# Performance work log

Measured on AMD Instinct MI355X. Metric: run time of the kernel, lower is better.

## Reference

```python
import jax, jax.numpy as jnp
import numpy as np

B, T = 64, 20
VOCAB, E, CE, ANS = 20000, 300, 1024, 3000
H, N, W, R = 512, 256, 64, 4
RW = R * W
IF_SIZES = [RW, R, W, 1, W, W, R, 1, 1, 3 * R]  # read_keys, read_str, write_key, write_str, erase, write_vec, free, alloc_g, write_g, modes
IF_TOT = sum(IF_SIZES)
CLIP = 20.0
EPS = 1e-6


def _cosine_weights(mem, keys, strengths):
    # mem [B,N,W], keys [B,K,W], strengths [B,K] -> softmax over N
    mem_n = mem / (jnp.linalg.norm(mem, axis=-1, keepdims=True) + EPS)
    key_n = keys / (jnp.linalg.norm(keys, axis=-1, keepdims=True) + EPS)
    sim = jnp.einsum('bkw,bnw->bkn', key_n, mem_n)
    return jax.nn.softmax(sim * strengths[..., None], axis=-1)


def _init_state(b):
    z = lambda *s: jnp.zeros(s, jnp.float32)
    return (z(b, N, W), z(b, N, N), z(b, N), z(b, R, N), z(b, N), z(b, N), z(b, R, W), z(b, H), z(b, H))


def _dnc_step(Wih, Whh, b, Wif, bif, Wout, bout, state, x):
    mem, link, prec, wr, ww, usage, rvec, h, c = state
    bsz = x.shape[0]
    inp = jnp.concatenate([x, rvec.reshape(bsz, RW)], -1)
    gates = inp @ Wih + h @ Whh + b
    gi, gf, gg, go = jnp.split(gates, 4, -1)
    c = jax.nn.sigmoid(gf) * c + jax.nn.sigmoid(gi) * jnp.tanh(gg)
    h = jax.nn.sigmoid(go) * jnp.tanh(c)
    hc = jnp.clip(h, -CLIP, CLIP)
    xi = hc @ Wif + bif
    p = jnp.split(xi, np.cumsum(IF_SIZES)[:-1].tolist(), axis=-1)
    read_keys = jnp.tanh(p[0]).reshape(bsz, R, W)
    read_str = jax.nn.softplus(p[1])
    write_key = jnp.tanh(p[2]).reshape(bsz, 1, W)
    write_str = jax.nn.softplus(p[3])
    erase = jax.nn.sigmoid(p[4])
    write_vec = jnp.tanh(p[5])
    free = jax.nn.sigmoid(p[6])
    alloc_g = jax.nn.sigmoid(p[7])
    write_g = jax.nn.sigmoid(p[8])
    modes = jax.nn.softmax(p[9].reshape(bsz, R, 3), -1)

    # usage update and allocation (sort-based, data dependent)
    psi = jnp.prod(1.0 - free[..., None] * wr, axis=1)          # [B,N]
    usage = (usage + ww - usage * ww) * psi
    s_idx = jnp.argsort(usage, axis=-1)                          # ascending usage
    s_u = jnp.take_along_axis(usage, s_idx, -1)
    cp = jnp.cumprod(jnp.concatenate([jnp.ones_like(s_u[:, :1]), s_u[:, :-1]], -1), -1)
    a_sorted = (1.0 - s_u) * cp
    inv = jnp.argsort(s_idx, axis=-1)
    alloc = jnp.take_along_axis(a_sorted, inv, -1)

    # write
    cw = _cosine_weights(mem, write_key, write_str)[:, 0]        # [B,N]
    ww = write_g * (alloc_g * alloc + (1.0 - alloc_g) * cw)
    mem = mem * (1.0 - ww[..., None] * erase[:, None, :]) + ww[..., None] * write_vec[:, None, :]

    # temporal link matrix
    link = (1.0 - ww[:, :, None] - ww[:, None, :]) * link + ww[:, :, None] * prec[:, None, :]
    link = link * (1.0 - jnp.eye(N, dtype=link.dtype))
    prec = (1.0 - ww.sum(-1, keepdims=True)) * prec + ww

    # read
    fw = jnp.einsum('bij,brj->bri', link, wr)
    bw = jnp.einsum('bji,brj->bri', link, wr)
    cr = _cosine_weights(mem, read_keys, read_str)
    wr = modes[..., 0:1] * bw + modes[..., 1:2] * cr + modes[..., 2:3] * fw
    rvec = jnp.einsum('brn,bnw->brw', wr, mem)

    out = jnp.concatenate([hc, rvec.reshape(bsz, RW)], -1) @ Wout + bout
    out = jnp.clip(out, -CLIP, CLIP)
    return (mem, link, prec, wr, ww, usage, rvec, h, c), out


def _model(img_feat, emb, img_W, img_b, q_Wih, q_Whh, q_b, q_Wif, q_bif, q_Wout, q_bout,
           c_Wih, c_Whh, c_b, c_Wif, c_bif, c_Wout, c_bout, fc1_W, fc1_b, fc2_W, fc2_b, qst):
    bsz = qst.shape[0]
    # question encoder: embedding -> tanh -> DNC over time -> mean pool
    qv = jnp.tanh(emb[qst])                                      # [B,T,E]
    step = lambda st, x: _dnc_step(q_Wih, q_Whh, q_b, q_Wif, q_bif, q_Wout, q_bout, st, x)
    _, outs = jax.lax.scan(step, _init_state(bsz), jnp.swapaxes(qv, 0, 1))
    qfeat = outs.mean(0)                                         # [B,CE]
    # image encoder: fc on frozen VGG feature, L2 norm (norm detached)
    imgf = img_feat @ img_W + img_b
    imgf = imgf / jax.lax.stop_gradient(jnp.linalg.norm(imgf, axis=1, keepdims=True))
    comb = jnp.tanh(imgf * qfeat)
    # controller DNC: single timestep
    st_c, out_c = _dnc_step(c_Wih, c_Whh, c_b, c_Wif, c_bif, c_Wout, c_bout, _init_state(bsz), comb)
    rv_c = st_c[6].reshape(bsz, RW)
    last = jnp.tanh(jnp.concatenate([out_c, rv_c], -1))
    last = jnp.tanh(last @ fc1_W + fc1_b)
    return last @ fc2_W + fc2_b                                  # logits [B,ANS]


def setup_inputs():
    ks = jax.random.split(jax.random.key(0), 20)
    g = lambda k, s, sc=0.05: jax.random.normal(k, s, dtype=jnp.float32) * sc
    z = lambda *s: jnp.zeros(s, jnp.float32)
    return {
        'img_feat': g(ks[0], (B, 4096), 1.0),
        'qst': jax.random.randint(ks[1], (B, T), 0, VOCAB),
        'emb': g(ks[2], (VOCAB, E)),
        'img_W': g(ks[3], (4096, CE)), 'img_b': z(CE),
        'q_Wih': g(ks[4], (E + RW, 4 * H)), 'q_Whh': g(ks[5], (H, 4 * H)), 'q_b': z(4 * H),
        'q_Wif': g(ks[6], (H, IF_TOT)), 'q_bif': z(IF_TOT),
        'q_Wout': g(ks[7], (H + RW, CE)), 'q_bout': z(CE),
        'c_Wih': g(ks[8], (CE + RW, 4 * H)), 'c_Whh': g(ks[9], (H, 4 * H)), 'c_b': z(4 * H),
        'c_Wif': g(ks[10], (H, IF_TOT)), 'c_bif': z(IF_TOT),
        'c_Wout': g(ks[11], (H + RW, CE)), 'c_bout': z(CE),
        'fc1_W': g(ks[12], (CE + RW, ANS)), 'fc1_b': z(ANS),
        'fc2_W': g(ks[13], (ANS, ANS)), 'fc2_b': z(ANS),
    }


def reference(img_feat, qst, emb, img_W, img_b, q_Wih, q_Whh, q_b, q_Wif, q_bif, q_Wout, q_bout,
              c_Wih, c_Whh, c_b, c_Wif, c_bif, c_Wout, c_bout, fc1_W, fc1_b, fc2_W, fc2_b):
    return _model(img_feat, emb, img_W, img_b, q_Wih, q_Whh, q_b, q_Wif, q_bif, q_Wout, q_bout,
                  c_Wih, c_Whh, c_b, c_Wif, c_bif, c_Wout, c_bout, fc1_W, fc1_b, fc2_W, fc2_b, qst)
```

## Files before the change

kernel.cpp:

```cpp
#include <hip/hip_runtime.h>
#include <cmath>

#define CLIPV 20.0f
#define EPSV 1e-6f

__device__ __forceinline__ float sigmoidf_(float x){ return 1.0f/(1.0f + expf(-x)); }
__device__ __forceinline__ float softplusf_(float x){ return (x > 20.0f) ? x : log1pf(expf(x)); }
__device__ __forceinline__ float clipf_(float x){ return fminf(fmaxf(x, -CLIPV), CLIPV); }

__device__ __forceinline__ float wave_sum64(float v){
  #pragma unroll
  for (int off=32; off>=1; off>>=1) v += __shfl_xor(v, off, 64);
  return v;
}
__device__ __forceinline__ float wave_max64(float v){
  #pragma unroll
  for (int off=32; off>=1; off>>=1) v = fmaxf(v, __shfl_xor(v, off, 64));
  return v;
}
__device__ __forceinline__ float block_sum256(float v, float* s_red){
  v = wave_sum64(v);
  __syncthreads();
  if ((threadIdx.x & 63) == 0) s_red[threadIdx.x>>6] = v;
  __syncthreads();
  return s_red[0]+s_red[1]+s_red[2]+s_red[3];
}
__device__ __forceinline__ float block_max256(float v, float* s_red){
  v = wave_max64(v);
  __syncthreads();
  if ((threadIdx.x & 63) == 0) s_red[threadIdx.x>>6] = v;
  __syncthreads();
  return fmaxf(fmaxf(s_red[0],s_red[1]), fmaxf(s_red[2],s_red[3]));
}

__device__ __forceinline__ void cstore(float* p, float v){
  __hip_atomic_store(p, v, __ATOMIC_RELAXED, __HIP_MEMORY_SCOPE_AGENT);
}

#define WS_MEM    0
#define WS_LINK   1048576
#define WS_PREC   5242880
#define WS_WR     5275648
#define WS_WW     5341184
#define WS_USAGE  5357568
#define WS_BAR    5373952
#define WS_ZONEA  5374976
#define WS_QSUM   5374976
#define WS_HTS    5440512
#define WS_RVS    6128640
#define WS_XIS    6472704
#define WS_GXP    7105728
#define WS_ZONEC  9727168
#define WS_IMGF   10879168
#define WS_COMB   10944704
#define WS_LASTB  11010240
#define WS_HID1   11092160
#define WS_QV     11284160

__global__ void embed_kernel(const int* __restrict__ qst, const float* __restrict__ emb,
                             float* __restrict__ qv){
  int idx = blockIdx.x*256 + threadIdx.x;
  if (idx >= 1280*300) return;
  int m = idx / 300;
  int e = idx - m*300;
  int t = m >> 6, b = m & 63;
  int tok = qst[b*20 + t];
  qv[idx] = tanhf(emb[(size_t)tok*300 + e]);
}

__global__ __launch_bounds__(256) void gemm64(
    int M, int N, int Ktot, int KS,
    const float* __restrict__ A, int lda,
    const float* __restrict__ B,
    const float* __restrict__ bias,
    float* __restrict__ out, float* __restrict__ part, int mode)
{
  __shared__ float As[32*68];
  __shared__ float Bs[32*68];
  int tid = threadIdx.x;
  int nb = blockIdx.x*64, ks = blockIdx.y, mb = blockIdx.z*64;
  int Kc = (((Ktot + KS - 1)/KS) + 3) & ~3;
  int kbeg = ks*Kc, kend = min(Ktot, kbeg + Kc);
  int tm = tid >> 4, tn = tid & 15;
  float acc[4][4];
  #pragma unroll
  for (int i=0;i<4;i++){ acc[i][0]=0.f; acc[i][1]=0.f; acc[i][2]=0.f; acc[i][3]=0.f; }

  for (int k0 = kbeg; k0 < kend; k0 += 32){
    int klim = kend - k0; if (klim > 32) klim = 32;
    #pragma unroll
    for (int i=0;i<2;i++){
      int idx = tid + i*256;
      int m = idx >> 3, kq = (idx & 7) << 2;
      if (kq < klim){
        const float* ap = A + (size_t)(mb+m)*lda + k0 + kq;
        float4 v;
        if (kq + 3 < klim) v = *(const float4*)ap;
        else { v.x=ap[0]; v.y=(kq+1<klim)?ap[1]:0.f; v.z=(kq+2<klim)?ap[2]:0.f; v.w=0.f; }
        float* as = As + m;
        as[(kq+0)*68]=v.x; as[(kq+1)*68]=v.y; as[(kq+2)*68]=v.z; as[(kq+3)*68]=v.w;
      }
    }
    #pragma unroll
    for (int i=0;i<2;i++){
      int idx = tid + i*256;
      int kk = idx >> 4, nq = (idx & 15) << 2;
      int n = nb + nq;
      float4 v = {0.f,0.f,0.f,0.f};
      if (kk < klim && n < N){
        const float* bp = B + (size_t)(k0+kk)*N + n;
        if (n + 3 < N) v = *(const float4*)bp;
        else { v.x=bp[0]; v.y=(n+1<N)?bp[1]:0.f; v.z=(n+2<N)?bp[2]:0.f; }
      }
      *(float4*)(Bs + kk*68 + nq) = v;
    }
    __syncthreads();
    for (int kk = 0; kk < klim; kk++){
      float4 a = *(const float4*)(As + kk*68 + tm*4);
      float4 bv = *(const float4*)(Bs + kk*68 + tn*4);
      acc[0][0]+=a.x*bv.x; acc[0][1]+=a.x*bv.y; acc[0][2]+=a.x*bv.z; acc[0][3]+=a.x*bv.w;
      acc[1][0]+=a.y*bv.x; acc[1][1]+=a.y*bv.y; acc[1][2]+=a.y*bv.z; acc[1][3]+=a.y*bv.w;
      acc[2][0]+=a.z*bv.x; acc[2][1]+=a.z*bv.y; acc[2][2]+=a.z*bv.z; acc[2][3]+=a.z*bv.w;
      acc[3][0]+=a.w*bv.x; acc[3][1]+=a.w*bv.y; acc[3][2]+=a.w*bv.z; acc[3][3]+=a.w*bv.w;
    }
    __syncthreads();
  }

  #pragma unroll
  for (int i=0;i<4;i++){
    int m = tm*4 + i;
    #pragma unroll
    for (int j=0;j<4;j++){
      int n = nb + tn*4 + j;
      if (n < N){
        if (mode == 0){
          part[((size_t)(ks*64 + m))*N + n] = acc[i][j];
        } else {
          float v = acc[i][j] + (bias ? bias[n] : 0.f);
          if (mode == 2) v = tanhf(v);
          out[(size_t)(mb+m)*N + n] = v;
        }
      }
    }
  }
}

__global__ void reduce64(const float* __restrict__ part, int KS, int MN4, int N,
                         const float* __restrict__ bias, float* __restrict__ out, int mode){
  int idx = blockIdx.x*256 + threadIdx.x;
  if (idx >= MN4) return;
  int base = idx*4;
  int n = base % N;
  float4 s = {0.f,0.f,0.f,0.f};
  size_t stride = (size_t)MN4*4;
  for (int p=0;p<KS;p++){
    float4 t = *(const float4*)(part + (size_t)p*stride + base);
    s.x+=t.x; s.y+=t.y; s.z+=t.z; s.w+=t.w;
  }
  if (bias){
    float4 bb = *(const float4*)(bias + n);
    s.x+=bb.x; s.y+=bb.y; s.z+=bb.z; s.w+=bb.w;
  }
  if (mode == 1){ s.x=tanhf(s.x); s.y=tanhf(s.y); s.z=tanhf(s.z); s.w=tanhf(s.w); }
  *(float4*)(out + base) = s;
}

__global__ __launch_bounds__(256) void comb_kernel(const float* __restrict__ imgf,
                                                   const float* __restrict__ qsum,
                                                   float* __restrict__ comb){
  __shared__ float s_red[4];
  int b = blockIdx.x, tid = threadIdx.x;
  float ss = 0.f;
  for (int j = tid; j < 1024; j += 256){ float v = imgf[b*1024+j]; ss += v*v; }
  ss = wave_sum64(ss);
  if ((tid & 63) == 0) s_red[tid>>6] = ss;
  __syncthreads();
  float inv = 1.0f / sqrtf(s_red[0]+s_red[1]+s_red[2]+s_red[3]);
  for (int j = tid; j < 1024; j += 256)
    comb[b*1024+j] = tanhf(imgf[b*1024+j]*inv * qsum[b*1024+j]*0.05f);
}

__global__ void tanhrvec_kernel(const float* __restrict__ rvecT, float* __restrict__ lastB){
  int idx = blockIdx.x*256 + threadIdx.x;
  if (idx >= 16384) return;
  int b = idx & 63, i = idx >> 6;
  lastB[(size_t)b*1280 + 1024 + i] = tanhf(rvecT[i*64 + b]);
}

struct SD_t {
  float s_rk[256], s_rstr[4], s_wkey[64], s_erase[64], s_wvec[64];
  float s_free[4], s_modes[12], s_scal[3], s_pad0[1];
  float s_wr[1024];
  float s_wwnew[256], s_usage[256], s_prec[256], s_scan[256], s_sim[256];
  float s_C[1024], s_D[1024];
  float s_red[4], s_PQ[8];
};
struct SGLO_t { float red[4*768]; float g2[768]; };
struct Shm {
  float Wg[768*8];
  float Wo[768*4];
  float Wi[512*4];
  union { SGLO_t glo; SD_t d; } u;
};


__device__ __forceinline__ void gbar(int* subs, int* root, int* ggen, int epoch){
  __syncthreads();
  if (threadIdx.x == 0){
    asm volatile("s_waitcnt vmcnt(0)" ::: "memory");
    int g = blockIdx.x & 15;
    int old = __hip_atomic_fetch_add(&subs[g*16], 1, __ATOMIC_RELAXED, __HIP_MEMORY_SCOPE_AGENT);
    if (old == 16*epoch - 1){
      int r = __hip_atomic_fetch_add(root, 1, __ATOMIC_RELAXED, __HIP_MEMORY_SCOPE_AGENT);
      if (r == 16*epoch - 1){
        #pragma unroll
        for (int gg = 0; gg < 16; gg++)
          __hip_atomic_store(&ggen[gg*16], epoch, __ATOMIC_RELAXED, __HIP_MEMORY_SCOPE_AGENT);
      }
    }
    while (__hip_atomic_load(&ggen[g*16], __ATOMIC_RELAXED, __HIP_MEMORY_SCOPE_AGENT) < epoch)
      __builtin_amdgcn_s_sleep(2);
    asm volatile("" ::: "memory");
  }
  __syncthreads();
}

__global__ __launch_bounds__(256) void dnc_recur(
    int T, int outmode, int slot0,
    const float* __restrict__ xpart, const float* __restrict__ Wih_r,
    const float* __restrict__ Whh, const float* __restrict__ gb,
    const float* __restrict__ Wif, const float* __restrict__ bif,
    const float* __restrict__ Wout, const float* __restrict__ bout,
    float* __restrict__ ws, float* __restrict__ outbuf, int* __restrict__ barmem)
{
  __shared__ Shm sh;

  float* memS  = ws + WS_MEM;
  float* linkS = ws + WS_LINK;
  float* precB = ws + WS_PREC;
  float* wrS   = ws + WS_WR;
  float* wwS   = ws + WS_WW;
  float* usgS  = ws + WS_USAGE;
  float* htS   = ws + WS_HTS;
  float* rvS   = ws + WS_RVS;
  float* xiSl  = ws + WS_XIS;
  int* subs  = barmem;
  int* root  = barmem + 256;
  int* ggen  = barmem + 288;
  int* xict  = barmem + 576;
  int* subsH = barmem + 608;
  int* rootH = barmem + 896;

  int tid = threadIdx.x, bid = blockIdx.x;
  int lane = tid & 63, wid = tid >> 6;
  int b_ = tid & 63, q_ = tid >> 6;

  {
    int c2 = bid*2;
    float2* Wg2w = (float2*)sh.Wg;
    for (int e2 = tid; e2 < 3072; e2 += 256){
      int k = e2 >> 2, g = e2 & 3;
      const float* src = (k < 256) ? (Wih_r + (size_t)k*2048 + g*512 + c2)
                                   : (Whh + (size_t)(k-256)*2048 + g*512 + c2);
      Wg2w[e2] = *(const float2*)src;
    }
    int c4o = bid*4;
    float4* Wo4 = (float4*)sh.Wo;
    for (int k = tid; k < 768; k += 256)
      Wo4[k] = *(const float4*)(Wout + (size_t)k*1024 + c4o);
    if (bid < 118){
      for (int e = tid; e < 2048; e += 256){
        int k = e >> 2, c = e & 3;
        int col = c4o + c;
        sh.Wi[e] = (col < 471) ? Wif[(size_t)k*471 + col] : 0.f;
      }
    }
  }
  float bo = bout[bid*4 + q_];
  float bifv = 0.f;
  if (bid < 118 && bid*4 + q_ < 471) bifv = bif[bid*4 + q_];
  __syncthreads();

  float c_reg = 0.f;
  float qacc = 0.f;
  int epoch = 0;

  for (int t = 0; t < T; t++){
    int pp = t & 1, wp = (t + 1) & 1;

    {
      if (t > 0){
        float accG[8] = {0.f,0.f,0.f,0.f,0.f,0.f,0.f,0.f};
        float accO[4] = {0.f,0.f,0.f,0.f};
        const float* rvP = rvS + (size_t)(slot0+t-1)*16384;
        const float* hP  = htS + (size_t)(slot0+t-1)*32768;
        for (int c = 0; c < 12; c++){
          int k0 = c*64 + wid*16;
          bool isH = (k0 >= 256);
          const float* src = isH ? (hP + (size_t)(k0-256)*64) : (rvP + (size_t)k0*64);
          float a[16];
          #pragma unroll
          for (int u=0; u<16; u++) a[u] = src[u*64 + lane];
          #pragma unroll
          for (int u=0; u<16; u++){
            int k = k0 + u;
            float4 w0 = *(const float4*)(sh.Wg + (size_t)k*8);
            float4 w1 = *(const float4*)(sh.Wg + (size_t)k*8 + 4);
            int orow = isH ? (k - 256) : (512 + k);
            float4 wo = *(const float4*)(sh.Wo + (size_t)orow*4);
            float av = a[u];
            float ao = isH ? clipf_(av) : av;
            accG[0] += av*w0.x; accG[1] += av*w0.y; accG[2] += av*w0.z; accG[3] += av*w0.w;
            accG[4] += av*w1.x; accG[5] += av*w1.y; accG[6] += av*w1.z; accG[7] += av*w1.w;
            accO[0] += ao*wo.x; accO[1] += ao*wo.y; accO[2] += ao*wo.z; accO[3] += ao*wo.w;
          }
        }
        #pragma unroll
        for (int j=0;j<8;j++) sh.u.glo.red[wid*768 + j*64 + lane] = accG[j];
        #pragma unroll
        for (int j=0;j<4;j++) sh.u.glo.red[wid*768 + (8+j)*64 + lane] = accO[j];
      }
      __syncthreads();
      #pragma unroll
      for (int v=0; v<3; v++){
        int j = q_ + v*4;
        float s;
        if (j < 8){
          int col = (j>>1)*512 + bid*2 + (j&1);
          s = gb[col] + xpart[((size_t)(t*64 + b_))*2048 + col];
        } else {
          s = bo;
        }
        if (t > 0){
          s += sh.u.glo.red[0*768 + j*64 + b_];
          s += sh.u.glo.red[1*768 + j*64 + b_];
          s += sh.u.glo.red[2*768 + j*64 + b_];
          s += sh.u.glo.red[3*768 + j*64 + b_];
        }
        sh.u.glo.g2[j*64 + b_] = s;
      }
      __syncthreads();
      if (t > 0) qacc += clipf_(sh.u.glo.g2[(8+q_)*64 + b_]);
      if (tid < 128){
        int jj = q_;
        float gi = sh.u.glo.g2[(0+jj)*64 + b_];
        float gf = sh.u.glo.g2[(2+jj)*64 + b_];
        float gg = sh.u.glo.g2[(4+jj)*64 + b_];
        float go = sh.u.glo.g2[(6+jj)*64 + b_];
        float cn = sigmoidf_(gf)*c_reg + sigmoidf_(gi)*tanhf(gg);
        float hn = sigmoidf_(go)*tanhf(cn);
        c_reg = cn;
        int col = bid*2 + jj;
        cstore(&htS[(size_t)(slot0+t)*32768 + col*64 + b_], hn);
      }
    }

    __syncthreads();
    if (tid == 0){
      asm volatile("s_waitcnt vmcnt(0)" ::: "memory");
      int g = bid & 15;
      int old = __hip_atomic_fetch_add(&subsH[g*16], 1, __ATOMIC_RELAXED, __HIP_MEMORY_SCOPE_AGENT);
      if (old == 16*(t+1) - 1)
        __hip_atomic_fetch_add(rootH, 1, __ATOMIC_RELAXED, __HIP_MEMORY_SCOPE_AGENT);
    }

    if (bid < 118){
      if (tid == 0){
        while (__hip_atomic_load(rootH, __ATOMIC_RELAXED, __HIP_MEMORY_SCOPE_AGENT) < 16*(t+1))
          __builtin_amdgcn_s_sleep(1);
        asm volatile("" ::: "memory");
      }
      __syncthreads();
      float acc[4] = {0.f,0.f,0.f,0.f};
      const float* hP = htS + (size_t)(slot0+t)*32768;
      for (int c = 0; c < 8; c++){
        int k0 = c*64 + wid*16;
        float a[16];
        #pragma unroll
        for (int u=0; u<16; u++) a[u] = hP[(size_t)(k0+u)*64 + lane];
        #pragma unroll
        for (int u=0; u<16; u++){
          float4 wv = *(const float4*)(sh.Wi + (size_t)(k0+u)*4);
          float ac = clipf_(a[u]);
          acc[0] += ac*wv.x; acc[1] += ac*wv.y; acc[2] += ac*wv.z; acc[3] += ac*wv.w;
        }
      }
      #pragma unroll
      for (int j=0;j<4;j++) sh.u.glo.red[wid*256 + j*64 + lane] = acc[j];
      __syncthreads();
      {
        float s = bifv;
        #pragma unroll
        for (int w=0;w<4;w++) s += sh.u.glo.red[w*256 + q_*64 + b_];
        int col = bid*4 + q_;
        if (col < 471) cstore(&xiSl[(size_t)(slot0+t)*30144 + b_*471 + col], s);
      }
      __syncthreads();
      if (tid == 0)
        __hip_atomic_fetch_add(xict, 1, __ATOMIC_RELAXED, __HIP_MEMORY_SCOPE_AGENT);
    }

    if (bid < 64){
      SD_t& sd = sh.u.d;
      int b = bid;
      const float* prec_in  = precB + pp*16384;
      float*       prec_out = precB + wp*16384;

      for (int e = tid; e < 1024; e += 256){
        sd.s_wr[e] = wrS[(size_t)b*1024 + e];
        sd.s_C[e] = 0.f; sd.s_D[e] = 0.f;
      }
      float wwold = wwS[(size_t)b*256 + tid];
      sd.s_usage[tid] = usgS[(size_t)b*256 + tid];
      sd.s_prec[tid]  = prec_in[(size_t)b*256 + tid];

      if (tid == 0){
        while (__hip_atomic_load(xict, __ATOMIC_RELAXED, __HIP_MEMORY_SCOPE_AGENT) < 118*(t+1))
          __builtin_amdgcn_s_sleep(1);
        asm volatile("" ::: "memory");
      }
      __syncthreads();

      const float* xrow = xiSl + (size_t)(slot0+t)*30144 + (size_t)b*471;
      for (int idx = tid; idx < 471; idx += 256){
        float v = xrow[idx];
        if (idx < 256)       sd.s_rk[idx] = tanhf(v);
        else if (idx < 260)  sd.s_rstr[idx-256] = softplusf_(v);
        else if (idx < 324)  sd.s_wkey[idx-260] = v;
        else if (idx == 324) sd.s_scal[0] = softplusf_(v);
        else if (idx < 389)  sd.s_erase[idx-325] = sigmoidf_(v);
        else if (idx < 453)  sd.s_wvec[idx-389] = tanhf(v);
        else if (idx < 457)  sd.s_free[idx-453] = sigmoidf_(v);
        else if (idx == 457) sd.s_scal[1] = sigmoidf_(v);
        else if (idx == 458) sd.s_scal[2] = sigmoidf_(v);
        else                 sd.s_modes[idx-459] = v;
      }
      __syncthreads();

      if (tid < 4){
        float m0 = sd.s_modes[tid*3], m1 = sd.s_modes[tid*3+1], m2 = sd.s_modes[tid*3+2];
        float mx = fmaxf(m0, fmaxf(m1,m2));
        float e0 = expf(m0-mx), e1 = expf(m1-mx), e2 = expf(m2-mx);
        float s = e0+e1+e2;
        sd.s_modes[tid*3] = e0/s; sd.s_modes[tid*3+1] = e1/s; sd.s_modes[tid*3+2] = e2/s;
      }
      {
        float k = sd.s_rk[wid*64 + lane];
        float ss = wave_sum64(k*k);
        sd.s_rk[wid*64 + lane] = k / (sqrtf(ss) + EPSV);
      }
      if (wid == 0){
        float k = sd.s_wkey[lane];
        float ss = wave_sum64(k*k);
        sd.s_wkey[lane] = k / (sqrtf(ss) + EPSV);
      }

      {
        float psi = 1.f;
        #pragma unroll
        for (int r=0;r<4;r++) psi *= (1.f - sd.s_free[r]*sd.s_wr[r*256+tid]);
        float u = (sd.s_usage[tid] + wwold - sd.s_usage[tid]*wwold) * psi;
        sd.s_usage[tid] = u;
        usgS[(size_t)b*256 + tid] = u;
      }
      __syncthreads();

      int rank_r;
      {
        float u = sd.s_usage[tid];
        int rank = 0;
        #pragma unroll 4
        for (int j4=0;j4<256;j4+=4){
          float4 uv = *(const float4*)(sd.s_usage + j4);
          rank += (uv.x < u) || (uv.x == u && (j4+0) < tid);
          rank += (uv.y < u) || (uv.y == u && (j4+1) < tid);
          rank += (uv.z < u) || (uv.z == u && (j4+2) < tid);
          rank += (uv.w < u) || (uv.w == u && (j4+3) < tid);
        }
        rank_r = rank;
        sd.s_scan[rank] = u;
      }
      __syncthreads();

      for (int off=1; off<256; off<<=1){
        float tv = (tid >= off) ? sd.s_scan[tid-off] : 1.f;
        __syncthreads();
        sd.s_scan[tid] *= tv;
        __syncthreads();
      }
      float alloc_r;
      {
        float u = sd.s_usage[tid];
        float cpe = (rank_r > 0) ? sd.s_scan[rank_r-1] : 1.f;
        alloc_r = (1.f - u) * cpe;
      }

      {
        const float4* Mrow = (const float4*)(memS + (size_t)b*16384 + (size_t)tid*64);
        float nrm2 = 0.f, dt = 0.f;
        #pragma unroll
        for (int c4 = 0; c4 < 16; c4++){
          float4 mv = Mrow[c4];
          int w0 = c4*4;
          nrm2 += mv.x*mv.x + mv.y*mv.y + mv.z*mv.z + mv.w*mv.w;
          dt += mv.x*sd.s_wkey[w0] + mv.y*sd.s_wkey[w0+1] + mv.z*sd.s_wkey[w0+2] + mv.w*sd.s_wkey[w0+3];
        }
        sd.s_sim[tid] = dt / (sqrtf(nrm2)+EPSV) * sd.s_scal[0];
      }
      __syncthreads();

      {
        float v = sd.s_sim[tid];
        float mx = block_max256(v, sd.s_red);
        float e = expf(v - mx);
        float sm = block_sum256(e, sd.s_red);
        float cw = e / sm;
        float wwn = sd.s_scal[2] * (sd.s_scal[1]*alloc_r + (1.f - sd.s_scal[1])*cw);
        sd.s_wwnew[tid] = wwn;
        wwS[(size_t)b*256 + tid] = wwn;
        float wws = block_sum256(wwn, sd.s_red);
        prec_out[(size_t)b*256 + tid] = (1.f - wws)*sd.s_prec[tid] + wwn;
        #pragma unroll
        for (int r=0;r<4;r++){
          float pv  = block_sum256(sd.s_prec[tid]*sd.s_wr[r*256+tid], sd.s_red);
          float qv_ = block_sum256(wwn*sd.s_wr[r*256+tid], sd.s_red);
          if (tid == 0){ sd.s_PQ[r] = pv; sd.s_PQ[4+r] = qv_; }
        }
      }
      __syncthreads();

      float aA[4] = {0,0,0,0}, aB[4] = {0,0,0,0};
      {
        const float4* Lrow = (const float4*)(linkS + (size_t)b*65536 + (size_t)tid*256);
        for (int c4 = 0; c4 < 64; c4++){
          float4 lv = Lrow[c4];
          int j = c4*4;
          float w0n = sd.s_wwnew[j], w1n = sd.s_wwnew[j+1], w2n = sd.s_wwnew[j+2], w3n = sd.s_wwnew[j+3];
          #pragma unroll
          for (int r=0;r<4;r++){
            float wr0 = sd.s_wr[r*256+j], wr1 = sd.s_wr[r*256+j+1];
            float wr2 = sd.s_wr[r*256+j+2], wr3 = sd.s_wr[r*256+j+3];
            aA[r] += lv.x*wr0 + lv.y*wr1 + lv.z*wr2 + lv.w*wr3;
            aB[r] += lv.x*(w0n*wr0) + lv.y*(w1n*wr1) + lv.z*(w2n*wr2) + lv.w*(w3n*wr3);
          }
        }
      }
      __syncthreads();

      {
        int cg = tid & 63, ioff = tid >> 6;
        int j0 = cg*4;
        float wwj0 = sd.s_wwnew[j0], wwj1 = sd.s_wwnew[j0+1], wwj2 = sd.s_wwnew[j0+2], wwj3 = sd.s_wwnew[j0+3];
        float pj0 = sd.s_prec[j0], pj1 = sd.s_prec[j0+1], pj2 = sd.s_prec[j0+2], pj3 = sd.s_prec[j0+3];
        float cC[4][4] = {{0}}, cD[4][4] = {{0}};
        float4* Lb = (float4*)(linkS + (size_t)b*65536);
        for (int it = 0; it < 64; it++){
          int i = it*4 + ioff;
          float4 lv = Lb[(size_t)i*64 + cg];
          float wwi = sd.s_wwnew[i];
          float4 ln;
          ln.x = (1.f - wwi - wwj0)*lv.x + wwi*pj0;
          ln.y = (1.f - wwi - wwj1)*lv.y + wwi*pj1;
          ln.z = (1.f - wwi - wwj2)*lv.z + wwi*pj2;
          ln.w = (1.f - wwi - wwj3)*lv.w + wwi*pj3;
          if (i >= j0 && i < j0+4){
            if (i == j0)        ln.x = 0.f;
            else if (i == j0+1) ln.y = 0.f;
            else if (i == j0+2) ln.z = 0.f;
            else                ln.w = 0.f;
          }
          Lb[(size_t)i*64 + cg] = ln;
          #pragma unroll
          for (int r=0;r<4;r++){
            float wri = sd.s_wr[r*256+i];
            float vbi = wwi*wri;
            cC[r][0] += lv.x*wri; cC[r][1] += lv.y*wri; cC[r][2] += lv.z*wri; cC[r][3] += lv.w*wri;
            cD[r][0] += lv.x*vbi; cD[r][1] += lv.y*vbi; cD[r][2] += lv.z*vbi; cD[r][3] += lv.w*vbi;
          }
        }
        for (int w=0; w<4; w++){
          if (ioff == w){
            #pragma unroll
            for (int r=0;r<4;r++){
              sd.s_C[r*256+j0+0] += cC[r][0]; sd.s_C[r*256+j0+1] += cC[r][1];
              sd.s_C[r*256+j0+2] += cC[r][2]; sd.s_C[r*256+j0+3] += cC[r][3];
              sd.s_D[r*256+j0+0] += cD[r][0]; sd.s_D[r*256+j0+1] += cD[r][1];
              sd.s_D[r*256+j0+2] += cD[r][2]; sd.s_D[r*256+j0+3] += cD[r][3];
            }
          }
          __syncthreads();
        }
      }

      float pr[4];
      {
        float4* Mrow = (float4*)(memS + (size_t)b*16384 + (size_t)tid*64);
        float wwn = sd.s_wwnew[tid];
        float nrm2 = 0.f, d0=0.f, d1=0.f, d2=0.f, d3=0.f;
        #pragma unroll
        for (int c4 = 0; c4 < 16; c4++){
          float4 mv = Mrow[c4];
          int w0 = c4*4;
          mv.x = mv.x*(1.f - wwn*sd.s_erase[w0+0]) + wwn*sd.s_wvec[w0+0];
          mv.y = mv.y*(1.f - wwn*sd.s_erase[w0+1]) + wwn*sd.s_wvec[w0+1];
          mv.z = mv.z*(1.f - wwn*sd.s_erase[w0+2]) + wwn*sd.s_wvec[w0+2];
          mv.w = mv.w*(1.f - wwn*sd.s_erase[w0+3]) + wwn*sd.s_wvec[w0+3];
          Mrow[c4] = mv;
          nrm2 += mv.x*mv.x + mv.y*mv.y + mv.z*mv.z + mv.w*mv.w;
          d0 += mv.x*sd.s_rk[w0] + mv.y*sd.s_rk[w0+1] + mv.z*sd.s_rk[w0+2] + mv.w*sd.s_rk[w0+3];
          d1 += mv.x*sd.s_rk[64+w0] + mv.y*sd.s_rk[64+w0+1] + mv.z*sd.s_rk[64+w0+2] + mv.w*sd.s_rk[64+w0+3];
          d2 += mv.x*sd.s_rk[128+w0] + mv.y*sd.s_rk[128+w0+1] + mv.z*sd.s_rk[128+w0+2] + mv.w*sd.s_rk[128+w0+3];
          d3 += mv.x*sd.s_rk[192+w0] + mv.y*sd.s_rk[192+w0+1] + mv.z*sd.s_rk[192+w0+2] + mv.w*sd.s_rk[192+w0+3];
        }
        float inv = 1.f/(sqrtf(nrm2)+EPSV);
        pr[0] = d0*inv*sd.s_rstr[0];
        pr[1] = d1*inv*sd.s_rstr[1];
        pr[2] = d2*inv*sd.s_rstr[2];
        pr[3] = d3*inv*sd.s_rstr[3];
      }
      #pragma unroll
      for (int r=0;r<4;r++){
        float mx = block_max256(pr[r], sd.s_red);
        float e = expf(pr[r] - mx);
        float sm = block_sum256(e, sd.s_red);
        pr[r] = e/sm;
      }
      __syncthreads();

      {
        float wwn = sd.s_wwnew[tid], pn = sd.s_prec[tid];
        #pragma unroll
        for (int r=0;r<4;r++){
          float wro = sd.s_wr[r*256+tid];
          float fw  = (1.f-wwn)*aA[r] - aB[r] + wwn*(sd.s_PQ[r] - pn*wro);
          float bwv = (1.f-wwn)*sd.s_C[r*256+tid] - sd.s_D[r*256+tid] + pn*(sd.s_PQ[4+r] - wwn*wro);
          float wrn = sd.s_modes[r*3+0]*bwv + sd.s_modes[r*3+1]*pr[r] + sd.s_modes[r*3+2]*fw;
          wrS[(size_t)b*1024 + r*256 + tid] = wrn;
          sd.s_wr[r*256+tid] = wrn;
        }
      }
      __syncthreads();

      {
        int r = tid >> 6, w = tid & 63;
        const float* Mb = memS + (size_t)b*16384;
        float acc = 0.f;
        for (int n=0; n<256; n++) acc += sd.s_wr[r*256+n]*Mb[(size_t)n*64 + w];
        cstore(&rvS[(size_t)(slot0+t)*16384 + (r*64 + w)*64 + b], acc);
      }
    }

    epoch++; gbar(subs, root, ggen, epoch);
  }

  {
    float accO[4] = {0.f,0.f,0.f,0.f};
    const float* rvP = rvS + (size_t)(slot0+T-1)*16384;
    const float* hP  = htS + (size_t)(slot0+T-1)*32768;
    for (int c = 0; c < 12; c++){
      int k0 = c*64 + wid*16;
      bool isH = (k0 >= 256);
      const float* src = isH ? (hP + (size_t)(k0-256)*64) : (rvP + (size_t)k0*64);
      float a[16];
      #pragma unroll
      for (int u=0; u<16; u++) a[u] = src[u*64 + lane];
      #pragma unroll
      for (int u=0; u<16; u++){
        int k = k0 + u;
        int orow = isH ? (k - 256) : (512 + k);
        float4 wo = *(const float4*)(sh.Wo + (size_t)orow*4);
        float av = isH ? clipf_(a[u]) : a[u];
        accO[0] += av*wo.x; accO[1] += av*wo.y; accO[2] += av*wo.z; accO[3] += av*wo.w;
      }
    }
    #pragma unroll
    for (int j=0;j<4;j++) sh.u.glo.red[wid*256 + j*64 + lane] = accO[j];
    __syncthreads();
    float v = bo;
    #pragma unroll
    for (int w=0;w<4;w++) v += sh.u.glo.red[w*256 + q_*64 + b_];
    v = clipf_(v);
    if (outmode == 0){
      qacc += v;
      outbuf[(size_t)b_*1024 + (bid*4 + q_)] = qacc;
    } else {
      outbuf[(size_t)b_*1280 + (bid*4 + q_)] = tanhf(v);
    }
  }
}

extern "C" void kernel_launch(void* const* d_in, const int* in_sizes, int n_in,
                              void* d_out, int out_size, void* d_ws, size_t ws_size,
                              hipStream_t stream) {
  const float* img_feat = (const float*)d_in[0];
  const int*   qst      = (const int*)  d_in[1];
  const float* emb      = (const float*)d_in[2];
  const float* img_W    = (const float*)d_in[3];
  const float* img_b    = (const float*)d_in[4];
  const float* q_Wih    = (const float*)d_in[5];
  const float* q_Whh    = (const float*)d_in[6];
  const float* q_b      = (const float*)d_in[7];
  const float* q_Wif    = (const float*)d_in[8];
  const float* q_bif    = (const float*)d_in[9];
  const float* q_Wout   = (const float*)d_in[10];
  const float* q_bout   = (const float*)d_in[11];
  const float* c_Wih    = (const float*)d_in[12];
  const float* c_Whh    = (const float*)d_in[13];
  const float* c_b      = (const float*)d_in[14];
  const float* c_Wif    = (const float*)d_in[15];
  const float* c_bif    = (const float*)d_in[16];
  const float* c_Wout   = (const float*)d_in[17];
  const float* c_bout   = (const float*)d_in[18];
  const float* fc1_W    = (const float*)d_in[19];
  const float* fc1_b    = (const float*)d_in[20];
  const float* fc2_W    = (const float*)d_in[21];
  const float* fc2_b    = (const float*)d_in[22];

  float* ws = (float*)d_ws;
  float* qv    = ws + WS_QV;
  float* gxp   = ws + WS_GXP;
  float* zoneC = ws + WS_ZONEC;
  float* imgf  = ws + WS_IMGF;
  float* combB = ws + WS_COMB;
  float* lastB = ws + WS_LASTB;
  float* hid1  = ws + WS_HID1;
  float* qsum  = ws + WS_QSUM;
  int*   bar   = (int*)(ws + WS_BAR);

  hipMemsetAsync(ws, 0, (size_t)WS_ZONEA*4, stream);

  embed_kernel<<<1500, 256, 0, stream>>>(qst, emb, qv);

  gemm64<<<dim3(16,16,1), 256, 0, stream>>>(64, 1024, 4096, 16,
      img_feat, 4096, img_W, nullptr, nullptr, zoneC, 0);
  reduce64<<<64, 256, 0, stream>>>(zoneC, 16, 16384, 1024, img_b, imgf, 0);

  gemm64<<<dim3(32,1,20), 256, 0, stream>>>(1280, 2048, 300, 1,
      qv, 300, q_Wih, nullptr, gxp, nullptr, 1);

  dnc_recur<<<256, 256, 0, stream>>>(20, 0, 0,
      gxp, q_Wih + (size_t)300*2048, q_Whh, q_b,
      q_Wif, q_bif, q_Wout, q_bout, ws, qsum, bar);

  comb_kernel<<<64, 256, 0, stream>>>(imgf, qsum, combB);

  hipMemsetAsync(ws, 0, (size_t)WS_ZONEA*4, stream);

  gemm64<<<dim3(32,4,1), 256, 0, stream>>>(64, 2048, 1024, 4,
      combB, 1024, c_Wih, nullptr, nullptr, zoneC, 0);
  reduce64<<<128, 256, 0, stream>>>(zoneC, 4, 32768, 2048, nullptr, gxp, 0);

  dnc_recur<<<256, 256, 0, stream>>>(1, 1, 20,
      gxp, c_Wih + (size_t)1024*2048, c_Whh, c_b,
      c_Wif, c_bif, c_Wout, c_bout, ws, lastB, bar);

  tanhrvec_kernel<<<64, 256, 0, stream>>>(ws + WS_RVS + (size_t)20*16384, lastB);

  gemm64<<<dim3(47,5,1), 256, 0, stream>>>(64, 3000, 1280, 5,
      lastB, 1280, fc1_W, nullptr, nullptr, zoneC, 0);
  reduce64<<<188, 256, 0, stream>>>(zoneC, 5, 48000, 3000, fc1_b, hid1, 1);

  gemm64<<<dim3(47,6,1), 256, 0, stream>>>(64, 3000, 3000, 6,
      hid1, 3000, fc2_W, nullptr, nullptr, zoneC, 0);
  reduce64<<<188, 256, 0, stream>>>(zoneC, 6, 48000, 3000, fc2_b, (float*)d_out, 0);
}
```

Measured before the change: 2.134 ms.

## Overlap h-part gate matmul with memory step and replace grid barrier with counter

Splits the per-step gate/output projection so the hidden-state contribution is computed right after h is published, into a new shared Pg buffer, instead of after the memory step. The DNC memory work moves to a separate block range (138..201), so it can run alongside the projection blocks. The full grid barrier is replaced by a read-vector completion counter that every block polls. It also batches block reductions (multi-value sum/max), rewrites the cumprod scan with wave shuffles, and replaces serialized C/D accumulation with per-wave partial buffers. The larger shared memory footprint may reduce occupancy, and the counter-based sync depends on the new barmem slot being zeroed.

```diff
diff --git a/kernel.cpp b/kernel.cpp
--- a/kernel.cpp
+++ b/kernel.cpp
@@ -31,6 +31,34 @@
   if ((threadIdx.x & 63) == 0) s_red[threadIdx.x>>6] = v;
   __syncthreads();
   return fmaxf(fmaxf(s_red[0],s_red[1]), fmaxf(s_red[2],s_red[3]));
+}
+template<int N>
+__device__ __forceinline__ void block_sumN(float (&v)[N], float* scr){
+  #pragma unroll
+  for (int i=0;i<N;i++) v[i] = wave_sum64(v[i]);
+  __syncthreads();
+  if ((threadIdx.x & 63) == 0){
+    int w = threadIdx.x >> 6;
+    #pragma unroll
+    for (int i=0;i<N;i++) scr[w*N + i] = v[i];
+  }
+  __syncthreads();
+  #pragma unroll
+  for (int i=0;i<N;i++) v[i] = scr[0*N+i] + scr[1*N+i] + scr[2*N+i] + scr[3*N+i];
+}
+template<int N>
+__device__ __forceinline__ void block_maxN(float (&v)[N], float* scr){
+  #pragma unroll
+  for (int i=0;i<N;i++) v[i] = wave_max64(v[i]);
+  __syncthreads();
+  if ((threadIdx.x & 63) == 0){
+    int w = threadIdx.x >> 6;
+    #pragma unroll
+    for (int i=0;i<N;i++) scr[w*N + i] = v[i];
+  }
+  __syncthreads();
+  #pragma unroll
+  for (int i=0;i<N;i++) v[i] = fmaxf(fmaxf(scr[0*N+i],scr[1*N+i]), fmaxf(scr[2*N+i],scr[3*N+i]));
 }
 
 __device__ __forceinline__ void cstore(float* p, float v){
@@ -187,43 +215,28 @@
   lastB[(size_t)b*1280 + 1024 + i] = tanhf(rvecT[i*64 + b]);
 }
 
+#define D_LO 138
+#define D_HI 202
+
 struct SD_t {
-  float s_rk[256], s_rstr[4], s_wkey[64], s_erase[64], s_wvec[64];
-  float s_free[4], s_modes[12], s_scal[3], s_pad0[1];
   float s_wr[1024];
+  float s_Cp[4096];
+  float s_Dp[4096];
+  float s_rk[256];
   float s_wwnew[256], s_usage[256], s_prec[256], s_scan[256], s_sim[256];
-  float s_C[1024], s_D[1024];
-  float s_red[4], s_PQ[8];
+  float s_wkey[64], s_erase[64], s_wvec[64];
+  float s_red[40];
+  float s_rstr[4], s_free[4], s_modes[12], s_scal[3];
 };
 struct SGLO_t { float red[4*768]; float g2[768]; };
 struct Shm {
   float Wg[768*8];
   float Wo[768*4];
   float Wi[512*4];
+  float Pg[4*768];
   union { SGLO_t glo; SD_t d; } u;
 };
 
-
-__device__ __forceinline__ void gbar(int* subs, int* root, int* ggen, int epoch){
-  __syncthreads();
-  if (threadIdx.x == 0){
-    asm volatile("s_waitcnt vmcnt(0)" ::: "memory");
-    int g = blockIdx.x & 15;
-    int old = __hip_atomic_fetch_add(&subs[g*16], 1, __ATOMIC_RELAXED, __HIP_MEMORY_SCOPE_AGENT);
-    if (old == 16*epoch - 1){
-      int r = __hip_atomic_fetch_add(root, 1, __ATOMIC_RELAXED, __HIP_MEMORY_SCOPE_AGENT);
-      if (r == 16*epoch - 1){
-        #pragma unroll
-        for (int gg = 0; gg < 16; gg++)
-          __hip_atomic_store(&ggen[gg*16], epoch, __ATOMIC_RELAXED, __HIP_MEMORY_SCOPE_AGENT);
-      }
-    }
-    while (__hip_atomic_load(&ggen[g*16], __ATOMIC_RELAXED, __HIP_MEMORY_SCOPE_AGENT) < epoch)
-      __builtin_amdgcn_s_sleep(2);
-    asm volatile("" ::: "memory");
-  }
-  __syncthreads();
-}
 
 __global__ __launch_bounds__(256) void dnc_recur(
     int T, int outmode, int slot0,
@@ -244,16 +257,15 @@
   float* htS   = ws + WS_HTS;
   float* rvS   = ws + WS_RVS;
   float* xiSl  = ws + WS_XIS;
-  int* subs  = barmem;
-  int* root  = barmem + 256;
-  int* ggen  = barmem + 288;
   int* xict  = barmem + 576;
   int* subsH = barmem + 608;
   int* rootH = barmem + 896;
+  int* rvct  = barmem + 928;
 
   int tid = threadIdx.x, bid = blockIdx.x;
   int lane = tid & 63, wid = tid >> 6;
   int b_ = tid & 63, q_ = tid >> 6;
+  bool isD = (bid >= D_LO && bid < D_HI);
 
   {
     int c2 = bid*2;
@@ -283,7 +295,6 @@
 
   float c_reg = 0.f;
   float qacc = 0.f;
-  int epoch = 0;
 
   for (int t = 0; t < T; t++){
     int pp = t & 1, wp = (t + 1) & 1;
@@ -293,11 +304,10 @@
         float accG[8] = {0.f,0.f,0.f,0.f,0.f,0.f,0.f,0.f};
         float accO[4] = {0.f,0.f,0.f,0.f};
         const float* rvP = rvS + (size_t)(slot0+t-1)*16384;
-        const float* hP  = htS + (size_t)(slot0+t-1)*32768;
-        for (int c = 0; c < 12; c++){
+        #pragma unroll
+        for (int c = 0; c < 4; c++){
           int k0 = c*64 + wid*16;
-          bool isH = (k0 >= 256);
-          const float* src = isH ? (hP + (size_t)(k0-256)*64) : (rvP + (size_t)k0*64);
+          const float* src = rvP + (size_t)k0*64;
           float a[16];
           #pragma unroll
           for (int u=0; u<16; u++) a[u] = src[u*64 + lane];
@@ -306,13 +316,11 @@
             int k = k0 + u;
             float4 w0 = *(const float4*)(sh.Wg + (size_t)k*8);
             float4 w1 = *(const float4*)(sh.Wg + (size_t)k*8 + 4);
-            int orow = isH ? (k - 256) : (512 + k);
-            float4 wo = *(const float4*)(sh.Wo + (size_t)orow*4);
+            float4 wo = *(const float4*)(sh.Wo + (size_t)(512 + k)*4);
             float av = a[u];
-            float ao = isH ? clipf_(av) : av;
             accG[0] += av*w0.x; accG[1] += av*w0.y; accG[2] += av*w0.z; accG[3] += av*w0.w;
             accG[4] += av*w1.x; accG[5] += av*w1.y; accG[6] += av*w1.z; accG[7] += av*w1.w;
-            accO[0] += ao*wo.x; accO[1] += ao*wo.y; accO[2] += ao*wo.z; accO[3] += ao*wo.w;
+            accO[0] += av*wo.x; accO[1] += av*wo.y; accO[2] += av*wo.z; accO[3] += av*wo.w;
           }
         }
         #pragma unroll
@@ -323,9 +331,9 @@
       __syncthreads();
       #pragma unroll
       for (int v=0; v<3; v++){
-        int j = q_ + v*4;
+        int j = (v < 2) ? (q_ + v*4) : (8 + q_);
         float s;
-        if (j < 8){
+        if (v < 2){
           int col = (j>>1)*512 + bid*2 + (j&1);
           s = gb[col] + xpart[((size_t)(t*64 + b_))*2048 + col];
         } else {
@@ -336,6 +344,10 @@
           s += sh.u.glo.red[1*768 + j*64 + b_];
           s += sh.u.glo.red[2*768 + j*64 + b_];
           s += sh.u.glo.red[3*768 + j*64 + b_];
+          s += sh.Pg[0*768 + j*64 + b_];
+          s += sh.Pg[1*768 + j*64 + b_];
+          s += sh.Pg[2*768 + j*64 + b_];
+          s += sh.Pg[3*768 + j*64 + b_];
         }
         sh.u.glo.g2[j*64 + b_] = s;
       }
@@ -362,15 +374,13 @@
       int old = __hip_atomic_fetch_add(&subsH[g*16], 1, __ATOMIC_RELAXED, __HIP_MEMORY_SCOPE_AGENT);
       if (old == 16*(t+1) - 1)
         __hip_atomic_fetch_add(rootH, 1, __ATOMIC_RELAXED, __HIP_MEMORY_SCOPE_AGENT);
-    }
+      while (__hip_atomic_load(rootH, __ATOMIC_RELAXED, __HIP_MEMORY_SCOPE_AGENT) < 16*(t+1))
+        __builtin_amdgcn_s_sleep(1);
+      asm volatile("" ::: "memory");
+    }
+    __syncthreads();
 
     if (bid < 118){
-      if (tid == 0){
-        while (__hip_atomic_load(rootH, __ATOMIC_RELAXED, __HIP_MEMORY_SCOPE_AGENT) < 16*(t+1))
-          __builtin_amdgcn_s_sleep(1);
-        asm volatile("" ::: "memory");
-      }
-      __syncthreads();
       float acc[4] = {0.f,0.f,0.f,0.f};
       const float* hP = htS + (size_t)(slot0+t)*32768;
       for (int c = 0; c < 8; c++){
@@ -400,16 +410,44 @@
         __hip_atomic_fetch_add(xict, 1, __ATOMIC_RELAXED, __HIP_MEMORY_SCOPE_AGENT);
     }
 
-    if (bid < 64){
+    {
+      const float* hP = htS + (size_t)(slot0+t)*32768;
+      float accG[8] = {0.f,0.f,0.f,0.f,0.f,0.f,0.f,0.f};
+      float accO[4] = {0.f,0.f,0.f,0.f};
+      #pragma unroll
+      for (int c = 4; c < 12; c++){
+        int k0 = c*64 + wid*16;
+        const float* src = hP + (size_t)(k0-256)*64;
+        float a[16];
+        #pragma unroll
+        for (int u=0; u<16; u++) a[u] = src[u*64 + lane];
+        #pragma unroll
+        for (int u=0; u<16; u++){
+          int k = k0 + u;
+          float4 w0 = *(const float4*)(sh.Wg + (size_t)k*8);
+          float4 w1 = *(const float4*)(sh.Wg + (size_t)k*8 + 4);
+          float4 wo = *(const float4*)(sh.Wo + (size_t)(k-256)*4);
+          float av = a[u];
+          float ao = clipf_(av);
+          accG[0] += av*w0.x; accG[1] += av*w0.y; accG[2] += av*w0.z; accG[3] += av*w0.w;
+          accG[4] += av*w1.x; accG[5] += av*w1.y; accG[6] += av*w1.z; accG[7] += av*w1.w;
+          accO[0] += ao*wo.x; accO[1] += ao*wo.y; accO[2] += ao*wo.z; accO[3] += ao*wo.w;
+        }
+      }
+      #pragma unroll
+      for (int j=0;j<8;j++) sh.Pg[wid*768 + j*64 + lane] = accG[j];
+      #pragma unroll
+      for (int j=0;j<4;j++) sh.Pg[wid*768 + (8+j)*64 + lane] = accO[j];
+    }
+
+    if (isD){
       SD_t& sd = sh.u.d;
-      int b = bid;
+      int b = bid - D_LO;
       const float* prec_in  = precB + pp*16384;
       float*       prec_out = precB + wp*16384;
 
-      for (int e = tid; e < 1024; e += 256){
+      for (int e = tid; e < 1024; e += 256)
         sd.s_wr[e] = wrS[(size_t)b*1024 + e];
-        sd.s_C[e] = 0.f; sd.s_D[e] = 0.f;
-      }
       float wwold = wwS[(size_t)b*256 + tid];
       sd.s_usage[tid] = usgS[(size_t)b*256 + tid];
       sd.s_prec[tid]  = prec_in[(size_t)b*256 + tid];
@@ -482,10 +520,21 @@
       }
       __syncthreads();
 
-      for (int off=1; off<256; off<<=1){
-        float tv = (tid >= off) ? sd.s_scan[tid-off] : 1.f;
+      {
+        float v = sd.s_scan[tid];
+        #pragma unroll
+        for (int off=1; off<64; off<<=1){
+          float u2 = __shfl_up(v, off, 64);
+          if (lane >= off) v *= u2;
+        }
+        if (lane == 63) sd.s_red[wid] = v;
         __syncthreads();
-        sd.s_scan[tid] *= tv;
+        float pre = 1.f;
+        if (wid > 0) pre *= sd.s_red[0];
+        if (wid > 1) pre *= sd.s_red[1];
+        if (wid > 2) pre *= sd.s_red[2];
+        v *= pre;
+        sd.s_scan[tid] = v;
         __syncthreads();
       }
       float alloc_r;
@@ -509,6 +558,7 @@
       }
       __syncthreads();
 
+      float pq[8];
       {
         float v = sd.s_sim[tid];
         float mx = block_max256(v, sd.s_red);
@@ -518,14 +568,16 @@
         float wwn = sd.s_scal[2] * (sd.s_scal[1]*alloc_r + (1.f - sd.s_scal[1])*cw);
         sd.s_wwnew[tid] = wwn;
         wwS[(size_t)b*256 + tid] = wwn;
-        float wws = block_sum256(wwn, sd.s_red);
-        prec_out[(size_t)b*256 + tid] = (1.f - wws)*sd.s_prec[tid] + wwn;
-        #pragma unroll
-        for (int r=0;r<4;r++){
-          float pv  = block_sum256(sd.s_prec[tid]*sd.s_wr[r*256+tid], sd.s_red);
-          float qv_ = block_sum256(wwn*sd.s_wr[r*256+tid], sd.s_red);
-          if (tid == 0){ sd.s_PQ[r] = pv; sd.s_PQ[4+r] = qv_; }
-        }
+        float r9[9];
+        r9[0] = wwn;
+        #pragma unroll
+        for (int r=0;r<4;r++) r9[1+r] = sd.s_prec[tid]*sd.s_wr[r*256+tid];
+        #pragma unroll
+        for (int r=0;r<4;r++) r9[5+r] = wwn*sd.s_wr[r*256+tid];
+        block_sumN<9>(r9, sd.s_red + 4);
+        prec_out[(size_t)b*256 + tid] = (1.f - r9[0])*sd.s_prec[tid] + wwn;
+        #pragma unroll
+        for (int r=0;r<4;r++){ pq[r] = r9[1+r]; pq[4+r] = r9[5+r]; }
       }
       __syncthreads();
 
@@ -547,6 +599,7 @@
       }
       __syncthreads();
 
+      float ccv[4], ddv[4];
       {
         int cg = tid & 63, ioff = tid >> 6;
         int j0 = cg*4;
@@ -578,17 +631,20 @@
             cD[r][0] += lv.x*vbi; cD[r][1] += lv.y*vbi; cD[r][2] += lv.z*vbi; cD[r][3] += lv.w*vbi;
           }
         }
-        for (int w=0; w<4; w++){
-          if (ioff == w){
-            #pragma unroll
-            for (int r=0;r<4;r++){
-              sd.s_C[r*256+j0+0] += cC[r][0]; sd.s_C[r*256+j0+1] += cC[r][1];
-              sd.s_C[r*256+j0+2] += cC[r][2]; sd.s_C[r*256+j0+3] += cC[r][3];
-              sd.s_D[r*256+j0+0] += cD[r][0]; sd.s_D[r*256+j0+1] += cD[r][1];
-              sd.s_D[r*256+j0+2] += cD[r][2]; sd.s_D[r*256+j0+3] += cD[r][3];
-            }
-          }
-          __syncthreads();
+        #pragma unroll
+        for (int r=0;r<4;r++){
+          float4 cv; cv.x=cC[r][0]; cv.y=cC[r][1]; cv.z=cC[r][2]; cv.w=cC[r][3];
+          float4 dv; dv.x=cD[r][0]; dv.y=cD[r][1]; dv.z=cD[r][2]; dv.w=cD[r][3];
+          *(float4*)(sd.s_Cp + ioff*1024 + r*256 + j0) = cv;
+          *(float4*)(sd.s_Dp + ioff*1024 + r*256 + j0) = dv;
+        }
+        __syncthreads();
+        #pragma unroll
+        for (int r=0;r<4;r++){
+          ccv[r] = sd.s_Cp[0*1024+r*256+tid] + sd.s_Cp[1*1024+r*256+tid]
+                 + sd.s_Cp[2*1024+r*256+tid] + sd.s_Cp[3*1024+r*256+tid];
+          ddv[r] = sd.s_Dp[0*1024+r*256+tid] + sd.s_Dp[1*1024+r*256+tid]
+                 + sd.s_Dp[2*1024+r*256+tid] + sd.s_Dp[3*1024+r*256+tid];
         }
       }
 
@@ -618,12 +674,16 @@
         pr[2] = d2*inv*sd.s_rstr[2];
         pr[3] = d3*inv*sd.s_rstr[3];
       }
-      #pragma unroll
-      for (int r=0;r<4;r++){
-        float mx = block_max256(pr[r], sd.s_red);
-        float e = expf(pr[r] - mx);
-        float sm = block_sum256(e, sd.s_red);
-        pr[r] = e/sm;
+      {
+        float m4[4] = {pr[0], pr[1], pr[2], pr[3]};
+        block_maxN<4>(m4, sd.s_red + 4);
+        float e4[4];
+        #pragma unroll
+        for (int r=0;r<4;r++) e4[r] = expf(pr[r] - m4[r]);
+        float s4[4] = {e4[0], e4[1], e4[2], e4[3]};
+        block_sumN<4>(s4, sd.s_red + 4);
+        #pragma unroll
+        for (int r=0;r<4;r++) pr[r] = e4[r]/s4[r];
       }
       __syncthreads();
 
@@ -632,8 +692,8 @@
         #pragma unroll
         for (int r=0;r<4;r++){
           float wro = sd.s_wr[r*256+tid];
-          float fw  = (1.f-wwn)*aA[r] - aB[r] + wwn*(sd.s_PQ[r] - pn*wro);
-          float bwv = (1.f-wwn)*sd.s_C[r*256+tid] - sd.s_D[r*256+tid] + pn*(sd.s_PQ[4+r] - wwn*wro);
+          float fw  = (1.f-wwn)*aA[r] - aB[r] + wwn*(pq[r] - pn*wro);
+          float bwv = (1.f-wwn)*ccv[r] - ddv[r] + pn*(pq[4+r] - wwn*wro);
           float wrn = sd.s_modes[r*3+0]*bwv + sd.s_modes[r*3+1]*pr[r] + sd.s_modes[r*3+2]*fw;
           wrS[(size_t)b*1024 + r*256 + tid] = wrn;
           sd.s_wr[r*256+tid] = wrn;
@@ -648,28 +708,37 @@
         for (int n=0; n<256; n++) acc += sd.s_wr[r*256+n]*Mb[(size_t)n*64 + w];
         cstore(&rvS[(size_t)(slot0+t)*16384 + (r*64 + w)*64 + b], acc);
       }
-    }
-
-    epoch++; gbar(subs, root, ggen, epoch);
+
+      __syncthreads();
+      if (tid == 0){
+        asm volatile("s_waitcnt vmcnt(0)" ::: "memory");
+        __hip_atomic_fetch_add(rvct, 1, __ATOMIC_RELAXED, __HIP_MEMORY_SCOPE_AGENT);
+      }
+    }
+
+    if (tid == 0){
+      while (__hip_atomic_load(rvct, __ATOMIC_RELAXED, __HIP_MEMORY_SCOPE_AGENT) < 64*(t+1))
+        __builtin_amdgcn_s_sleep(2);
+      asm volatile("" ::: "memory");
+    }
+    __syncthreads();
   }
 
   {
     float accO[4] = {0.f,0.f,0.f,0.f};
     const float* rvP = rvS + (size_t)(slot0+T-1)*16384;
-    const float* hP  = htS + (size_t)(slot0+T-1)*32768;
-    for (int c = 0; c < 12; c++){
+    #pragma unroll
+    for (int c = 0; c < 4; c++){
       int k0 = c*64 + wid*16;
-      bool isH = (k0 >= 256);
-      const float* src = isH ? (hP + (size_t)(k0-256)*64) : (rvP + (size_t)k0*64);
+      const float* src = rvP + (size_t)k0*64;
       float a[16];
       #pragma unroll
       for (int u=0; u<16; u++) a[u] = src[u*64 + lane];
       #pragma unroll
       for (int u=0; u<16; u++){
         int k = k0 + u;
-        int orow = isH ? (k - 256) : (512 + k);
-        float4 wo = *(const float4*)(sh.Wo + (size_t)orow*4);
-        float av = isH ? clipf_(a[u]) : a[u];
+        float4 wo = *(const float4*)(sh.Wo + (size_t)(512 + k)*4);
+        float av = a[u];
         accO[0] += av*wo.x; accO[1] += av*wo.y; accO[2] += av*wo.z; accO[3] += av*wo.w;
       }
     }
@@ -679,6 +748,8 @@
     float v = bo;
     #pragma unroll
     for (int w=0;w<4;w++) v += sh.u.glo.red[w*256 + q_*64 + b_];
+    #pragma unroll
+    for (int w=0;w<4;w++) v += sh.Pg[w*768 + (8+q_)*64 + b_];
     v = clipf_(v);
     if (outmode == 0){
       qacc += v;
```

New measurement: 3.433 ms. 60.9% more time.
